# Kernel optimization log

Measured on AMD Instinct MI355X. Metric: run time of the kernel, lower is better.

Reference implementation:

```python
import jax, jax.numpy as jnp
from jax import lax
import numpy as np

B, S, H = 4, 4096, 1024
NH, HD, L = 8, 128, 64
EPS = 1e-8


def setup_inputs() -> dict:
    key = jax.random.key(0)
    ks = jax.random.split(key, 11)
    std = 0.02
    d = NH * HD
    return {
        "f_in": jax.random.normal(ks[0], (B, S, H), jnp.float32),
        "i_in": jax.random.normal(ks[1], (B, S, H), jnp.float32),
        "z_in": jax.random.normal(ks[2], (B, S, H), jnp.float32),
        "o_in": jax.random.normal(ks[3], (B, S, H), jnp.float32),
        "c0": jax.random.normal(ks[4], (B, NH, HD), jnp.float32),
        "h0": jax.random.normal(ks[5], (B, NH, HD), jnp.float32),
        "Wf": jax.random.normal(ks[6], (d, H), jnp.float32) * std,
        "bf": jnp.zeros((d,), jnp.float32),
        "Wi": jax.random.normal(ks[7], (d, H), jnp.float32) * std,
        "bi": jnp.zeros((d,), jnp.float32),
        "Wz": jax.random.normal(ks[8], (d, H), jnp.float32) * std,
        "bz": jnp.zeros((d,), jnp.float32),
        "Wo": jax.random.normal(ks[9], (d, H), jnp.float32) * std,
        "bo": jnp.zeros((d,), jnp.float32),
        "Wp": jax.random.normal(ks[10], (H, d), jnp.float32) * std,
        "bp": jnp.zeros((H,), jnp.float32),
    }


def _to_blocks(x):
    # (B,S,NH*HD) -> (n_blocks, B, NH, HD, L)
    nb = S // L
    return x.reshape(B, nb, L, NH, HD).transpose(1, 0, 3, 4, 2)


def reference(f_in, i_in, z_in, o_in, c0, h0, Wf, bf, Wi, bi, Wz, bz, Wo, bo, Wp, bp):
    fx = _to_blocks(f_in @ Wf.T + bf)
    ix = _to_blocks(i_in @ Wi.T + bi)
    zx = _to_blocks(z_in @ Wz.T + bz)
    ox = _to_blocks(o_in @ Wo.T + bo)

    f = jax.nn.sigmoid(fx + 1.0)            # (nb,B,NH,HD,L)
    o = jax.nn.sigmoid(ox)
    upd = jax.nn.sigmoid(ix) * jnp.tanh(zx)

    k = jnp.arange(L)[:, None]
    l = jnp.arange(L + 1)[None, :]
    ones_mask = l >= k + 1                   # set to 1 before cumulative log-prod
    zeros_mask = l >= k + 2                  # strictly-future entries zeroed

    def block_step(c, blk):
        fb, ub, ob = blk                     # each (B,NH,HD,L)
        cf = jnp.concatenate(
            [fb, jnp.ones(fb.shape[:3] + (1,), fb.dtype)], axis=3)  # (B,NH,HD,L+1)
        Fm = jnp.broadcast_to(cf[:, :, :, None, :], fb.shape[:3] + (L, L + 1))
        Fm = jnp.where(ones_mask, 1.0, Fm)
        # reverse cumulative product in log space (matches torch eps trick)
        Fm = jnp.exp(jnp.flip(jnp.cumsum(jnp.flip(jnp.log(Fm + EPS), -1), -1), -1)) - EPS
        Fm = jnp.where(zeros_mask, 0.0, Fm)  # (B,NH,HD,L,L+1)
        u = jnp.concatenate([c[..., None], ub], axis=3)  # (B,NH,HD,L+1)
        cs = jnp.einsum('bhdkl,bhdl->bhdk', Fm, u)       # (B,NH,HD,L)
        hs = ob * jnp.tanh(cs)
        return cs[..., -1], hs

    last_c, hs = lax.scan(block_step, c0, (f, upd, o))   # hs: (nb,B,NH,HD,L)
    last_h = hs[-1][..., -1]
    y = hs.transpose(1, 0, 4, 2, 3).reshape(B, S, NH * HD)
    y = y @ Wp.T + bp                                    # (B,S,H)
    return y, last_c, last_h
```

## Files before the change

kernel.cpp:

```cpp
#include <hip/hip_runtime.h>
#include <hip/hip_bf16.h>
#include <type_traits>

#define GATE_ELEMS 16777216ull

typedef float f32x4 __attribute__((ext_vector_type(4)));
typedef short s16x8 __attribute__((ext_vector_type(8)));

__device__ __forceinline__ unsigned short f2bf(float f) {
  union { float f; unsigned u; } v; v.f = f;
  unsigned r = v.u + 0x7fffu + ((v.u >> 16) & 1u);
  return (unsigned short)(r >> 16);
}

__device__ __forceinline__ float bf2f(unsigned short u) {
  union { unsigned u; float f; } v; v.u = ((unsigned)u) << 16;
  return v.f;
}

__device__ __forceinline__ float sigmoidf_(float x) {
  return 1.0f / (1.0f + __expf(-x));
}

__device__ __forceinline__ float tanhf_(float x) {
  x = fminf(fmaxf(x, -15.f), 15.f);
  const float e = __expf(2.f * x);
  return (e - 1.f) / (e + 1.f);
}

template <typename AT, typename OT>
__global__ __launch_bounds__(256, 3)
void gemm_bt_kernel(const AT* __restrict__ A, const float* __restrict__ B,
                    const float* __restrict__ bias, OT* __restrict__ C,
                    int M, int N, int K) {
  __shared__ unsigned short As[128 * 40];
  __shared__ unsigned short Bs[128 * 40];
  const int tid  = threadIdx.x;
  const int lane = tid & 63;
  const int wave = tid >> 6;
  const int wr = wave >> 1;
  const int wc = wave & 1;
  const int m0 = blockIdx.y * 128;
  const int n0 = blockIdx.x * 128;

  f32x4 acc[4][4];
#pragma unroll
  for (int i = 0; i < 4; ++i)
#pragma unroll
    for (int j = 0; j < 4; ++j)
      acc[i][j] = (f32x4){0.f, 0.f, 0.f, 0.f};

  const int frow = lane & 15;
  const int kq   = lane >> 4;
  const int krow = kq * 8;

  for (int kt = 0; kt < K; kt += 32) {
    if constexpr (std::is_same<AT, float>::value) {
#pragma unroll
      for (int i = 0; i < 4; ++i) {
        const int fi  = (i * 256 + tid) * 4;
        const int row = fi >> 5;
        const int col = fi & 31;
        const float4 av = *reinterpret_cast<const float4*>(A + (size_t)(m0 + row) * K + kt + col);
        *reinterpret_cast<ushort4*>(&As[row * 40 + col]) =
            make_ushort4(f2bf(av.x), f2bf(av.y), f2bf(av.z), f2bf(av.w));
      }
    } else {
#pragma unroll
      for (int i = 0; i < 2; ++i) {
        const int fi  = (i * 256 + tid) * 8;
        const int row = fi >> 5;
        const int col = fi & 31;
        const s16x8 av = *reinterpret_cast<const s16x8*>(A + (size_t)(m0 + row) * K + kt + col);
        *reinterpret_cast<s16x8*>(&As[row * 40 + col]) = av;
      }
    }
#pragma unroll
    for (int i = 0; i < 4; ++i) {
      const int fi  = (i * 256 + tid) * 4;
      const int row = fi >> 5;
      const int col = fi & 31;
      const float4 bv = *reinterpret_cast<const float4*>(B + (size_t)(n0 + row) * K + kt + col);
      *reinterpret_cast<ushort4*>(&Bs[row * 40 + col]) =
          make_ushort4(f2bf(bv.x), f2bf(bv.y), f2bf(bv.z), f2bf(bv.w));
    }
    __syncthreads();

    s16x8 afr[4], bfr[4];
#pragma unroll
    for (int mf = 0; mf < 4; ++mf)
      afr[mf] = *reinterpret_cast<const s16x8*>(&As[(wr * 64 + mf * 16 + frow) * 40 + krow]);
#pragma unroll
    for (int nf = 0; nf < 4; ++nf)
      bfr[nf] = *reinterpret_cast<const s16x8*>(&Bs[(wc * 64 + nf * 16 + frow) * 40 + krow]);
#pragma unroll
    for (int mf = 0; mf < 4; ++mf)
#pragma unroll
      for (int nf = 0; nf < 4; ++nf)
        acc[mf][nf] = __builtin_amdgcn_mfma_f32_16x16x32_bf16(afr[mf], bfr[nf], acc[mf][nf], 0, 0, 0);
    __syncthreads();
  }

#pragma unroll
  for (int nf = 0; nf < 4; ++nf) {
    const int col = n0 + wc * 64 + nf * 16 + frow;
    const float bv = bias[col];
#pragma unroll
    for (int mf = 0; mf < 4; ++mf) {
      const int rbase = m0 + wr * 64 + mf * 16 + kq * 4;
#pragma unroll
      for (int r = 0; r < 4; ++r) {
        const float v = acc[mf][nf][r] + bv;
        if constexpr (std::is_same<OT, float>::value)
          C[(size_t)(rbase + r) * N + col] = v;
        else
          C[(size_t)(rbase + r) * N + col] = f2bf(v);
      }
    }
  }
}

__global__ void scan_pass1(const unsigned short* __restrict__ gates,
                           float* __restrict__ P, float* __restrict__ cl) {
  const int t = blockIdx.x * 256 + threadIdx.x;
  const int j = t & 1023;
  const int q = (t >> 10) & 63;
  const int b = t >> 16;
  const size_t base = ((size_t)(b * 4096 + q * 64)) * 1024 + j;
  const unsigned short* fx = gates;
  const unsigned short* ix = gates + GATE_ELEMS;
  const unsigned short* zx = gates + 2 * GATE_ELEMS;
  float Pp = 1.f, c = 0.f;
  for (int s = 0; s < 64; ++s) {
    const size_t o = base + (size_t)s * 1024;
    const float f = sigmoidf_(bf2f(fx[o]) + 1.f);
    const float u = sigmoidf_(bf2f(ix[o])) * tanhf_(bf2f(zx[o]));
    Pp *= f;
    c = f * c + u;
  }
  const int sidx = q * 4096 + b * 1024 + j;
  P[sidx]  = Pp;
  cl[sidx] = c;
}

__global__ void scan_pass2(const float* __restrict__ P, const float* __restrict__ cl,
                           const float* __restrict__ c0, float* __restrict__ cin,
                           float* __restrict__ lastc) {
  const int idx = blockIdx.x * 256 + threadIdx.x;
  float carry = c0[idx];
#pragma unroll
  for (int q = 0; q < 64; ++q) {
    const int s = q * 4096 + idx;
    cin[s] = carry;
    carry = fmaf(P[s], carry, cl[s]);
  }
  lastc[idx] = carry;
}

__global__ void scan_pass3(const unsigned short* __restrict__ gates,
                           const float* __restrict__ cin,
                           unsigned short* __restrict__ h,
                           float* __restrict__ lasth) {
  const int t = blockIdx.x * 256 + threadIdx.x;
  const int j = t & 1023;
  const int q = (t >> 10) & 63;
  const int b = t >> 16;
  const size_t base = ((size_t)(b * 4096 + q * 64)) * 1024 + j;
  const unsigned short* fx = gates;
  const unsigned short* ix = gates + GATE_ELEMS;
  const unsigned short* zx = gates + 2 * GATE_ELEMS;
  const unsigned short* ox = gates + 3 * GATE_ELEMS;
  float c = cin[q * 4096 + b * 1024 + j];
  float hv = 0.f;
  for (int s = 0; s < 64; ++s) {
    const size_t o = base + (size_t)s * 1024;
    const float f = sigmoidf_(bf2f(fx[o]) + 1.f);
    const float u = sigmoidf_(bf2f(ix[o])) * tanhf_(bf2f(zx[o]));
    c = f * c + u;
    hv = sigmoidf_(bf2f(ox[o])) * tanhf_(c);
    h[o] = f2bf(hv);
  }
  if (q == 63) lasth[b * 1024 + j] = hv;
}

extern "C" void kernel_launch(void* const* d_in, const int* in_sizes, int n_in,
                              void* d_out, int out_size, void* d_ws, size_t ws_size,
                              hipStream_t stream) {
  const float* xin[4]  = {(const float*)d_in[0], (const float*)d_in[1],
                          (const float*)d_in[2], (const float*)d_in[3]};
  const float* c0      = (const float*)d_in[4];
  const float* W[4]    = {(const float*)d_in[6], (const float*)d_in[8],
                          (const float*)d_in[10], (const float*)d_in[12]};
  const float* bias[4] = {(const float*)d_in[7], (const float*)d_in[9],
                          (const float*)d_in[11], (const float*)d_in[13]};
  const float* Wp = (const float*)d_in[14];
  const float* bp = (const float*)d_in[15];
  float* out = (float*)d_out;

  unsigned short* gates = (unsigned short*)d_ws;
  unsigned short* h     = gates + 4 * GATE_ELEMS;
  float* Pbuf   = (float*)(h + GATE_ELEMS);
  float* clbuf  = Pbuf + 262144;
  float* cinbuf = clbuf + 262144;

  const dim3 gg(8, 128, 1);
  for (int g = 0; g < 4; ++g)
    gemm_bt_kernel<float, unsigned short><<<gg, 256, 0, stream>>>(
        xin[g], W[g], bias[g], gates + (size_t)g * GATE_ELEMS, 16384, 1024, 1024);

  scan_pass1<<<1024, 256, 0, stream>>>(gates, Pbuf, clbuf);
  scan_pass2<<<16, 256, 0, stream>>>(Pbuf, clbuf, c0, cinbuf, out + GATE_ELEMS);
  scan_pass3<<<1024, 256, 0, stream>>>(gates, cinbuf, h, out + GATE_ELEMS + 4096);

  gemm_bt_kernel<unsigned short, float><<<gg, 256, 0, stream>>>(
      h, Wp, bp, out, 16384, 1024, 1024);
}
```

Measured before the change: 796.9 us.

## Preconvert inputs to bf16, use direct global-to-LDS loads, vectorize scans

Adds separate passes that convert activations and weights to bf16 once, so the GEMMs load bf16 tiles straight into LDS with global_load_lds rather than converting fp32 per tile. Blocks are remapped to a grouped order for cache locality. The scan kernels now process four channels per thread with vector loads and stores. Gate buffers reuse the output and the consumed input buffers. The costs are an extra conversion pass over all inputs and an unpadded LDS layout that may incur bank conflicts.

Result: faster. 671.1 us (-15.8%).

```diff
diff --git a/kernel.cpp b/kernel.cpp
--- a/kernel.cpp
+++ b/kernel.cpp
@@ -3,45 +3,85 @@
 #include <type_traits>
 
 #define GATE_ELEMS 16777216ull
+#define W_ELEMS    1048576ull
 
 typedef float f32x4 __attribute__((ext_vector_type(4)));
 typedef short s16x8 __attribute__((ext_vector_type(8)));
-
-__device__ __forceinline__ unsigned short f2bf(float f) {
+typedef unsigned short u16;
+
+__device__ __forceinline__ u16 f2bf(float f) {
   union { float f; unsigned u; } v; v.f = f;
   unsigned r = v.u + 0x7fffu + ((v.u >> 16) & 1u);
-  return (unsigned short)(r >> 16);
-}
-
-__device__ __forceinline__ float bf2f(unsigned short u) {
+  return (u16)(r >> 16);
+}
+__device__ __forceinline__ float bf2f(u16 u) {
   union { unsigned u; float f; } v; v.u = ((unsigned)u) << 16;
   return v.f;
 }
-
 __device__ __forceinline__ float sigmoidf_(float x) {
   return 1.0f / (1.0f + __expf(-x));
 }
-
 __device__ __forceinline__ float tanhf_(float x) {
   x = fminf(fmaxf(x, -15.f), 15.f);
   const float e = __expf(2.f * x);
   return (e - 1.f) / (e + 1.f);
 }
 
-template <typename AT, typename OT>
+__device__ __forceinline__ void load_lds16(const u16* g, u16* l) {
+  __builtin_amdgcn_global_load_lds(
+      (const __attribute__((address_space(1))) unsigned int*)g,
+      (__attribute__((address_space(3))) unsigned int*)l, 16, 0, 0);
+}
+
+__global__ void cvt_x_kernel(const float* __restrict__ x0, const float* __restrict__ x1,
+                             const float* __restrict__ x2, const float* __restrict__ x3,
+                             u16* __restrict__ dst) {
+  const float* src = (blockIdx.y == 0) ? x0 : (blockIdx.y == 1) ? x1
+                   : (blockIdx.y == 2) ? x2 : x3;
+  u16* d = dst + (size_t)blockIdx.y * GATE_ELEMS;
+  const size_t i = ((size_t)blockIdx.x * 256 + threadIdx.x) * 8;
+  const float4 a = *reinterpret_cast<const float4*>(src + i);
+  const float4 b = *reinterpret_cast<const float4*>(src + i + 4);
+  ushort4 lo = make_ushort4(f2bf(a.x), f2bf(a.y), f2bf(a.z), f2bf(a.w));
+  ushort4 hi = make_ushort4(f2bf(b.x), f2bf(b.y), f2bf(b.z), f2bf(b.w));
+  *reinterpret_cast<ushort4*>(d + i)     = lo;
+  *reinterpret_cast<ushort4*>(d + i + 4) = hi;
+}
+
+__global__ void cvt_w_kernel(const float* __restrict__ w0, const float* __restrict__ w1,
+                             const float* __restrict__ w2, const float* __restrict__ w3,
+                             const float* __restrict__ w4, u16* __restrict__ dst) {
+  const float* src = (blockIdx.y == 0) ? w0 : (blockIdx.y == 1) ? w1
+                   : (blockIdx.y == 2) ? w2 : (blockIdx.y == 3) ? w3 : w4;
+  u16* d = dst + (size_t)blockIdx.y * W_ELEMS;
+  const size_t i = ((size_t)blockIdx.x * 256 + threadIdx.x) * 8;
+  const float4 a = *reinterpret_cast<const float4*>(src + i);
+  const float4 b = *reinterpret_cast<const float4*>(src + i + 4);
+  ushort4 lo = make_ushort4(f2bf(a.x), f2bf(a.y), f2bf(a.z), f2bf(a.w));
+  ushort4 hi = make_ushort4(f2bf(b.x), f2bf(b.y), f2bf(b.z), f2bf(b.w));
+  *reinterpret_cast<ushort4*>(d + i)     = lo;
+  *reinterpret_cast<ushort4*>(d + i + 4) = hi;
+}
+
+template <typename OT>
 __global__ __launch_bounds__(256, 3)
-void gemm_bt_kernel(const AT* __restrict__ A, const float* __restrict__ B,
-                    const float* __restrict__ bias, OT* __restrict__ C,
-                    int M, int N, int K) {
-  __shared__ unsigned short As[128 * 40];
-  __shared__ unsigned short Bs[128 * 40];
+void gemm_bt_bf16(const u16* __restrict__ A, const u16* __restrict__ B,
+                  const float* __restrict__ bias, OT* __restrict__ C,
+                  int M, int N, int K) {
+  __shared__ __align__(16) u16 As[128 * 32];
+  __shared__ __align__(16) u16 Bs[128 * 32];
   const int tid  = threadIdx.x;
   const int lane = tid & 63;
   const int wave = tid >> 6;
   const int wr = wave >> 1;
   const int wc = wave & 1;
-  const int m0 = blockIdx.y * 128;
-  const int n0 = blockIdx.x * 128;
+
+  const int cpx = gridDim.x >> 3;
+  int bid = blockIdx.x;
+  bid = (bid & 7) * cpx + (bid >> 3);
+  const int nbx = N >> 7;
+  const int m0 = (bid / nbx) * 128;
+  const int n0 = (bid % nbx) * 128;
 
   f32x4 acc[4][4];
 #pragma unroll
@@ -54,45 +94,25 @@
   const int kq   = lane >> 4;
   const int krow = kq * 8;
 
+  const int lrow = lane >> 2;
+  const int lcol = (lane & 3) * 8;
+
   for (int kt = 0; kt < K; kt += 32) {
-    if constexpr (std::is_same<AT, float>::value) {
-#pragma unroll
-      for (int i = 0; i < 4; ++i) {
-        const int fi  = (i * 256 + tid) * 4;
-        const int row = fi >> 5;
-        const int col = fi & 31;
-        const float4 av = *reinterpret_cast<const float4*>(A + (size_t)(m0 + row) * K + kt + col);
-        *reinterpret_cast<ushort4*>(&As[row * 40 + col]) =
-            make_ushort4(f2bf(av.x), f2bf(av.y), f2bf(av.z), f2bf(av.w));
-      }
-    } else {
-#pragma unroll
-      for (int i = 0; i < 2; ++i) {
-        const int fi  = (i * 256 + tid) * 8;
-        const int row = fi >> 5;
-        const int col = fi & 31;
-        const s16x8 av = *reinterpret_cast<const s16x8*>(A + (size_t)(m0 + row) * K + kt + col);
-        *reinterpret_cast<s16x8*>(&As[row * 40 + col]) = av;
-      }
-    }
-#pragma unroll
-    for (int i = 0; i < 4; ++i) {
-      const int fi  = (i * 256 + tid) * 4;
-      const int row = fi >> 5;
-      const int col = fi & 31;
-      const float4 bv = *reinterpret_cast<const float4*>(B + (size_t)(n0 + row) * K + kt + col);
-      *reinterpret_cast<ushort4*>(&Bs[row * 40 + col]) =
-          make_ushort4(f2bf(bv.x), f2bf(bv.y), f2bf(bv.z), f2bf(bv.w));
+#pragma unroll
+    for (int i = 0; i < 2; ++i) {
+      const int rb = (i * 4 + wave) * 16;
+      load_lds16(A + (size_t)(m0 + rb + lrow) * K + kt + lcol, &As[rb * 32]);
+      load_lds16(B + (size_t)(n0 + rb + lrow) * K + kt + lcol, &Bs[rb * 32]);
     }
     __syncthreads();
 
     s16x8 afr[4], bfr[4];
 #pragma unroll
     for (int mf = 0; mf < 4; ++mf)
-      afr[mf] = *reinterpret_cast<const s16x8*>(&As[(wr * 64 + mf * 16 + frow) * 40 + krow]);
+      afr[mf] = *reinterpret_cast<const s16x8*>(&As[(wr * 64 + mf * 16 + frow) * 32 + krow]);
 #pragma unroll
     for (int nf = 0; nf < 4; ++nf)
-      bfr[nf] = *reinterpret_cast<const s16x8*>(&Bs[(wc * 64 + nf * 16 + frow) * 40 + krow]);
+      bfr[nf] = *reinterpret_cast<const s16x8*>(&Bs[(wc * 64 + nf * 16 + frow) * 32 + krow]);
 #pragma unroll
     for (int mf = 0; mf < 4; ++mf)
 #pragma unroll
@@ -120,27 +140,35 @@
   }
 }
 
-__global__ void scan_pass1(const unsigned short* __restrict__ gates,
+__global__ void scan_pass1(const u16* __restrict__ fx, const u16* __restrict__ ix,
+                           const u16* __restrict__ zx,
                            float* __restrict__ P, float* __restrict__ cl) {
-  const int t = blockIdx.x * 256 + threadIdx.x;
-  const int j = t & 1023;
-  const int q = (t >> 10) & 63;
-  const int b = t >> 16;
-  const size_t base = ((size_t)(b * 4096 + q * 64)) * 1024 + j;
-  const unsigned short* fx = gates;
-  const unsigned short* ix = gates + GATE_ELEMS;
-  const unsigned short* zx = gates + 2 * GATE_ELEMS;
-  float Pp = 1.f, c = 0.f;
+  const int t  = blockIdx.x * 256 + threadIdx.x;
+  const int jg = (t & 255) * 4;
+  const int q  = (t >> 8) & 63;
+  const int b  = t >> 14;
+  const size_t base = ((size_t)(b * 4096 + q * 64)) * 1024 + jg;
+  float Pp[4] = {1.f, 1.f, 1.f, 1.f};
+  float c[4]  = {0.f, 0.f, 0.f, 0.f};
   for (int s = 0; s < 64; ++s) {
     const size_t o = base + (size_t)s * 1024;
-    const float f = sigmoidf_(bf2f(fx[o]) + 1.f);
-    const float u = sigmoidf_(bf2f(ix[o])) * tanhf_(bf2f(zx[o]));
-    Pp *= f;
-    c = f * c + u;
-  }
-  const int sidx = q * 4096 + b * 1024 + j;
-  P[sidx]  = Pp;
-  cl[sidx] = c;
+    const ushort4 fv = *reinterpret_cast<const ushort4*>(fx + o);
+    const ushort4 iv = *reinterpret_cast<const ushort4*>(ix + o);
+    const ushort4 zv = *reinterpret_cast<const ushort4*>(zx + o);
+    const u16* fp = (const u16*)&fv;
+    const u16* ip = (const u16*)&iv;
+    const u16* zp = (const u16*)&zv;
+#pragma unroll
+    for (int k = 0; k < 4; ++k) {
+      const float f = sigmoidf_(bf2f(fp[k]) + 1.f);
+      const float u = sigmoidf_(bf2f(ip[k])) * tanhf_(bf2f(zp[k]));
+      Pp[k] *= f;
+      c[k] = f * c[k] + u;
+    }
+  }
+  const int sidx = q * 4096 + b * 1024 + jg;
+  *reinterpret_cast<float4*>(P + sidx)  = make_float4(Pp[0], Pp[1], Pp[2], Pp[3]);
+  *reinterpret_cast<float4*>(cl + sidx) = make_float4(c[0], c[1], c[2], c[3]);
 }
 
 __global__ void scan_pass2(const float* __restrict__ P, const float* __restrict__ cl,
@@ -157,30 +185,43 @@
   lastc[idx] = carry;
 }
 
-__global__ void scan_pass3(const unsigned short* __restrict__ gates,
+__global__ void scan_pass3(const u16* __restrict__ fx, const u16* __restrict__ ix,
+                           const u16* __restrict__ zx, const u16* __restrict__ ox,
                            const float* __restrict__ cin,
-                           unsigned short* __restrict__ h,
-                           float* __restrict__ lasth) {
-  const int t = blockIdx.x * 256 + threadIdx.x;
-  const int j = t & 1023;
-  const int q = (t >> 10) & 63;
-  const int b = t >> 16;
-  const size_t base = ((size_t)(b * 4096 + q * 64)) * 1024 + j;
-  const unsigned short* fx = gates;
-  const unsigned short* ix = gates + GATE_ELEMS;
-  const unsigned short* zx = gates + 2 * GATE_ELEMS;
-  const unsigned short* ox = gates + 3 * GATE_ELEMS;
-  float c = cin[q * 4096 + b * 1024 + j];
-  float hv = 0.f;
+                           u16* __restrict__ h, float* __restrict__ lasth) {
+  const int t  = blockIdx.x * 256 + threadIdx.x;
+  const int jg = (t & 255) * 4;
+  const int q  = (t >> 8) & 63;
+  const int b  = t >> 14;
+  const size_t base = ((size_t)(b * 4096 + q * 64)) * 1024 + jg;
+  const float4 ci = *reinterpret_cast<const float4*>(cin + q * 4096 + b * 1024 + jg);
+  float c[4]  = {ci.x, ci.y, ci.z, ci.w};
+  float hv[4] = {0.f, 0.f, 0.f, 0.f};
   for (int s = 0; s < 64; ++s) {
     const size_t o = base + (size_t)s * 1024;
-    const float f = sigmoidf_(bf2f(fx[o]) + 1.f);
-    const float u = sigmoidf_(bf2f(ix[o])) * tanhf_(bf2f(zx[o]));
-    c = f * c + u;
-    hv = sigmoidf_(bf2f(ox[o])) * tanhf_(c);
-    h[o] = f2bf(hv);
-  }
-  if (q == 63) lasth[b * 1024 + j] = hv;
+    const ushort4 fv = *reinterpret_cast<const ushort4*>(fx + o);
+    const ushort4 iv = *reinterpret_cast<const ushort4*>(ix + o);
+    const ushort4 zv = *reinterpret_cast<const ushort4*>(zx + o);
+    const ushort4 ov = *reinterpret_cast<const ushort4*>(ox + o);
+    const u16* fp = (const u16*)&fv;
+    const u16* ip = (const u16*)&iv;
+    const u16* zp = (const u16*)&zv;
+    const u16* op = (const u16*)&ov;
+    ushort4 hw;
+    u16* hp = (u16*)&hw;
+#pragma unroll
+    for (int k = 0; k < 4; ++k) {
+      const float f = sigmoidf_(bf2f(fp[k]) + 1.f);
+      const float u = sigmoidf_(bf2f(ip[k])) * tanhf_(bf2f(zp[k]));
+      c[k] = f * c[k] + u;
+      hv[k] = sigmoidf_(bf2f(op[k])) * tanhf_(c[k]);
+      hp[k] = f2bf(hv[k]);
+    }
+    *reinterpret_cast<ushort4*>(h + o) = hw;
+  }
+  if (q == 63)
+    *reinterpret_cast<float4*>(lasth + b * 1024 + jg) =
+        make_float4(hv[0], hv[1], hv[2], hv[3]);
 }
 
 extern "C" void kernel_launch(void* const* d_in, const int* in_sizes, int n_in,
@@ -189,29 +230,41 @@
   const float* xin[4]  = {(const float*)d_in[0], (const float*)d_in[1],
                           (const float*)d_in[2], (const float*)d_in[3]};
   const float* c0      = (const float*)d_in[4];
-  const float* W[4]    = {(const float*)d_in[6], (const float*)d_in[8],
-                          (const float*)d_in[10], (const float*)d_in[12]};
-  const float* bias[4] = {(const float*)d_in[7], (const float*)d_in[9],
-                          (const float*)d_in[11], (const float*)d_in[13]};
-  const float* Wp = (const float*)d_in[14];
-  const float* bp = (const float*)d_in[15];
+  const float* W[5]    = {(const float*)d_in[6], (const float*)d_in[8],
+                          (const float*)d_in[10], (const float*)d_in[12],
+                          (const float*)d_in[14]};
+  const float* bias[5] = {(const float*)d_in[7], (const float*)d_in[9],
+                          (const float*)d_in[11], (const float*)d_in[13],
+                          (const float*)d_in[15]};
   float* out = (float*)d_out;
 
-  unsigned short* gates = (unsigned short*)d_ws;
-  unsigned short* h     = gates + 4 * GATE_ELEMS;
-  float* Pbuf   = (float*)(h + GATE_ELEMS);
+  u16* xbf = (u16*)d_ws;
+  u16* wbf = xbf + 4 * GATE_ELEMS;
+  float* Pbuf   = (float*)(wbf + 5 * W_ELEMS);
   float* clbuf  = Pbuf + 262144;
   float* cinbuf = clbuf + 262144;
 
-  const dim3 gg(8, 128, 1);
+  u16* gp[4];
+  gp[0] = (u16*)d_out;
+  gp[1] = xbf;
+  gp[2] = xbf + GATE_ELEMS;
+  gp[3] = xbf + 2 * GATE_ELEMS;
+  u16* h = xbf + 3 * GATE_ELEMS;
+
+  cvt_x_kernel<<<dim3(8192, 4), 256, 0, stream>>>(xin[0], xin[1], xin[2], xin[3], xbf);
+  cvt_w_kernel<<<dim3(512, 5), 256, 0, stream>>>(W[0], W[1], W[2], W[3], W[4], wbf);
+
+  const dim3 gg(1024, 1, 1);
   for (int g = 0; g < 4; ++g)
-    gemm_bt_kernel<float, unsigned short><<<gg, 256, 0, stream>>>(
-        xin[g], W[g], bias[g], gates + (size_t)g * GATE_ELEMS, 16384, 1024, 1024);
-
-  scan_pass1<<<1024, 256, 0, stream>>>(gates, Pbuf, clbuf);
+    gemm_bt_bf16<u16><<<gg, 256, 0, stream>>>(
+        xbf + (size_t)g * GATE_ELEMS, wbf + (size_t)g * W_ELEMS, bias[g],
+        gp[g], 16384, 1024, 1024);
+
+  scan_pass1<<<256, 256, 0, stream>>>(gp[0], gp[1], gp[2], Pbuf, clbuf);
   scan_pass2<<<16, 256, 0, stream>>>(Pbuf, clbuf, c0, cinbuf, out + GATE_ELEMS);
-  scan_pass3<<<1024, 256, 0, stream>>>(gates, cinbuf, h, out + GATE_ELEMS + 4096);
-
-  gemm_bt_kernel<unsigned short, float><<<gg, 256, 0, stream>>>(
-      h, Wp, bp, out, 16384, 1024, 1024);
-}
+  scan_pass3<<<256, 256, 0, stream>>>(gp[0], gp[1], gp[2], gp[3], cinbuf, h,
+                                      out + GATE_ELEMS + 4096);
+
+  gemm_bt_bf16<float><<<gg, 256, 0, stream>>>(h, wbf + 4 * W_ELEMS, bias[4],
+                                              out, 16384, 1024, 1024);
+}
```
